# Performance work log

Hardware: AMD Instinct MI355X
Metric: run time of the kernel (lower is better)

The kernel has to match this reference:

```python
import jax, jax.numpy as jnp
import numpy as np

B, S, HID = 2, 2048, 4096
NH, NKV, D = 32, 8, 128  # heads, kv heads, head_dim
GROUPS = NH // NKV
THETA = 10000.0


def _rope_tables():
    inv_freq = 1.0 / (THETA ** (np.arange(0, D, 2, dtype=np.float32) / D))
    pos = np.arange(S, dtype=np.float32)
    freqs = pos[:, None] * inv_freq[None, :]          # [S, D/2]
    emb = np.concatenate([freqs, freqs], axis=-1)      # [S, D]
    cos = np.broadcast_to(np.cos(emb)[None], (B, S, D)).copy()
    sin = np.broadcast_to(np.sin(emb)[None], (B, S, D)).copy()
    return jnp.asarray(cos), jnp.asarray(sin)


def setup_inputs() -> dict:
    key = jax.random.key(0)
    ks = jax.random.split(key, 5)
    hidden_states = jax.random.normal(ks[0], (B, S, HID), dtype=jnp.float32)
    cos, sin = _rope_tables()
    std = 0.02
    Wq = jax.random.normal(ks[1], (NH * D, HID), dtype=jnp.float32) * std
    Wk = jax.random.normal(ks[2], (NKV * D, HID), dtype=jnp.float32) * std
    Wv = jax.random.normal(ks[3], (NKV * D, HID), dtype=jnp.float32) * std
    Wo = jax.random.normal(ks[4], (HID, NH * D), dtype=jnp.float32) * std
    return {"hidden_states": hidden_states, "cos": cos, "sin": sin,
            "Wq": Wq, "Wk": Wk, "Wv": Wv, "Wo": Wo}


def _rotate_half(x):
    x1, x2 = jnp.split(x, 2, axis=-1)
    return jnp.concatenate([-x2, x1], axis=-1)


def reference(hidden_states, cos, sin, Wq, Wk, Wv, Wo):
    b, s, _ = hidden_states.shape
    # QKV projections (no bias; attention_bias=False)
    q = (hidden_states @ Wq.T).reshape(b, s, NH, D).transpose(0, 2, 1, 3)    # [B,NH,S,D]
    k = (hidden_states @ Wk.T).reshape(b, s, NKV, D).transpose(0, 2, 1, 3)   # [B,NKV,S,D]
    v = (hidden_states @ Wv.T).reshape(b, s, NKV, D).transpose(0, 2, 1, 3)
    # RoPE (HF apply_rotary_pos_emb: cos/sin unsqueezed at head dim)
    c = cos[:, None, :, :]
    sn = sin[:, None, :, :]
    q = q * c + _rotate_half(q) * sn
    k = k * c + _rotate_half(k) * sn
    # GQA repeat_kv
    k = jnp.repeat(k, GROUPS, axis=1)                                        # [B,NH,S,D]
    v = jnp.repeat(v, GROUPS, axis=1)
    # dense evalmode: scores + causal mask + fp32 softmax
    scores = jnp.einsum('bhqd,bhkd->bhqk', q, k) / jnp.sqrt(jnp.float32(D))
    causal = jnp.triu(jnp.ones((s, s), dtype=bool), k=1)                     # True above diag
    scores = jnp.where(causal[None, None], jnp.float32(-jnp.inf), scores)
    attn = jax.nn.softmax(scores.astype(jnp.float32), axis=-1).astype(v.dtype)
    out = jnp.einsum('bhqk,bhkd->bhqd', attn, v)                             # [B,NH,S,D]
    out = out.transpose(0, 2, 1, 3).reshape(b, s, NH * D)
    return out @ Wo.T
```

## Files before the change

### kernel.cpp

```cpp
#include <hip/hip_runtime.h>
#include <hip/hip_bf16.h>

#define DEV __device__ __forceinline__

typedef __attribute__((ext_vector_type(8))) short bf16x8;
typedef __attribute__((ext_vector_type(4))) short s16x4;
typedef __attribute__((ext_vector_type(4))) float f32x4;

constexpr int B_ = 2, S_ = 2048, HID_ = 4096, NH_ = 32, NKV_ = 8, D_ = 128;
constexpr int GROUPS_ = NH_ / NKV_;
constexpr float QSCALE_ = 0.08838834764831845f * 1.4426950408889634f;

DEV unsigned short f2bf(float x) {
    union { float f; unsigned int u; } v; v.f = x;
    unsigned int r = v.u + 0x7fffu + ((v.u >> 16) & 1u);
    return (unsigned short)(r >> 16);
}

DEV f32x4 mfma16(bf16x8 a, bf16x8 b, f32x4 c) {
    return __builtin_amdgcn_mfma_f32_16x16x32_bf16(a, b, c, 0, 0, 0);
}

DEV void gll16(const void* g, void* l) {
    __builtin_amdgcn_global_load_lds(
        (const __attribute__((address_space(1))) unsigned int*)g,
        (__attribute__((address_space(3))) unsigned int*)l, 16, 0, 0);
}

__global__ __launch_bounds__(256) void cast_all_k(
    const float* __restrict__ s0, const float* __restrict__ s1,
    const float* __restrict__ s2, const float* __restrict__ s3,
    const float* __restrict__ s4,
    unsigned short* __restrict__ d0, unsigned short* __restrict__ d1,
    unsigned short* __restrict__ d2, unsigned short* __restrict__ d3,
    unsigned short* __restrict__ d4)
{
    int bb = blockIdx.x;
    const float* s; unsigned short* d; int off;
    if      (bb < 8192)  { s = s0; d = d0; off = bb; }
    else if (bb < 16384) { s = s1; d = d1; off = bb - 8192; }
    else if (bb < 18432) { s = s2; d = d2; off = bb - 16384; }
    else if (bb < 20480) { s = s3; d = d3; off = bb - 18432; }
    else                 { s = s4; d = d4; off = bb - 20480; }
    size_t i = ((size_t)off * 256 + threadIdx.x) * 8;
    const f32x4* sp = (const f32x4*)(s + i);
    f32x4 a = sp[0], b = sp[1];
    bf16x8 o;
    o[0] = (short)f2bf(a[0]); o[1] = (short)f2bf(a[1]);
    o[2] = (short)f2bf(a[2]); o[3] = (short)f2bf(a[3]);
    o[4] = (short)f2bf(b[0]); o[5] = (short)f2bf(b[1]);
    o[6] = (short)f2bf(b[2]); o[7] = (short)f2bf(b[3]);
    *(bf16x8*)(d + i) = o;
}

template<int EPI>
__global__ __launch_bounds__(512, 2) void gemm256_k(
    const unsigned short* __restrict__ A, const unsigned short* __restrict__ Bw,
    float* __restrict__ Cf, unsigned short* __restrict__ Qo,
    const float* __restrict__ cosT, const float* __restrict__ sinT,
    int M, int N, int K)
{
    __shared__ __align__(16) unsigned short lds[65536];
    const int tid = threadIdx.x, lane = tid & 63;
    const int w = tid >> 6, wm = w >> 2, wn = w & 3;
    const int la = lane & 15, lb = lane >> 4;

    const int nwg = (int)gridDim.x;
    const int cpx = nwg >> 3;
    const int bid = (int)blockIdx.x;
    const int sw = (bid & 7) * cpx + (bid >> 3);
    const int ntn = N >> 8;
    const int bm = (sw / ntn) << 8, bn = (sw % ntn) << 8;

    const int srow = tid >> 3;
    const int scol8 = (tid & 7) ^ (srow & 7);
    const size_t rK = (size_t)K;
    const unsigned short* gA = A + (size_t)(bm + srow) * rK + scol8 * 8;
    const unsigned short* gB = Bw + (size_t)(bn + srow) * rK + scol8 * 8;

#define STAGE_A_H0(buf, kt) { gll16(gA + (size_t)(kt),            &lds[(buf)*16384 + tid*8]); \
                              gll16(gA + (size_t)(kt) + 128*rK,   &lds[(buf)*16384 + 8192 + tid*8]); }
#define STAGE_A_H1(buf, kt) { gll16(gA + (size_t)(kt) + 64*rK,    &lds[(buf)*16384 + 4096 + tid*8]); \
                              gll16(gA + (size_t)(kt) + 192*rK,   &lds[(buf)*16384 + 12288 + tid*8]); }
#define STAGE_B_H0(buf, kt) { gll16(gB + (size_t)(kt),            &lds[32768 + (buf)*16384 + tid*8]); \
                              gll16(gB + (size_t)(kt) + 64*rK,    &lds[32768 + (buf)*16384 + 4096 + tid*8]); }
#define STAGE_B_H1(buf, kt) { gll16(gB + (size_t)(kt) + 128*rK,   &lds[32768 + (buf)*16384 + 8192 + tid*8]); \
                              gll16(gB + (size_t)(kt) + 192*rK,   &lds[32768 + (buf)*16384 + 12288 + tid*8]); }
#define SB0() __builtin_amdgcn_sched_barrier(0)

    f32x4 acc[8][4];
#pragma unroll
    for (int m = 0; m < 8; ++m)
#pragma unroll
        for (int j = 0; j < 4; ++j) acc[m][j] = f32x4{0.f, 0.f, 0.f, 0.f};

    auto rdA = [&](int buf, int m, int kk) -> bf16x8 {
        int r = wm * 128 + m * 16 + la;
        int slot = (kk * 4 + lb) ^ (la & 7);
        return *(const bf16x8*)&lds[buf * 16384 + r * 64 + slot * 8];
    };
    auto rdB = [&](int buf, int j, int kk) -> bf16x8 {
        int r = (wn + 4 * j) * 16 + la;
        int slot = (kk * 4 + lb) ^ (la & 7);
        return *(const bf16x8*)&lds[32768 + buf * 16384 + r * 64 + slot * 8];
    };

    STAGE_A_H0(0, 0); STAGE_B_H0(0, 0); STAGE_B_H1(0, 0); STAGE_A_H1(0, 0);

    bf16x8 af[4][2], b01[2][2], b23[2][2];
    int cur = 0;
    const int nt = K >> 6;
    for (int t = 0; t < nt; ++t) {
        const bool pre = (t + 1 < nt);
        const int kn = (t + 1) << 6;
        const int nb = cur ^ 1;
        asm volatile("s_waitcnt vmcnt(2)" ::: "memory");
        SB0(); __builtin_amdgcn_s_barrier(); SB0();
#pragma unroll
        for (int m = 0; m < 4; ++m)
#pragma unroll
            for (int kk = 0; kk < 2; ++kk) af[m][kk] = rdA(cur, m, kk);
#pragma unroll
        for (int j = 0; j < 2; ++j)
#pragma unroll
            for (int kk = 0; kk < 2; ++kk) b01[j][kk] = rdB(cur, j, kk);
        if (pre) STAGE_A_H0(nb, kn);
        __builtin_amdgcn_s_setprio(1);
#pragma unroll
        for (int kk = 0; kk < 2; ++kk)
#pragma unroll
            for (int m = 0; m < 4; ++m)
#pragma unroll
                for (int j = 0; j < 2; ++j)
                    acc[m][j] = mfma16(af[m][kk], b01[j][kk], acc[m][j]);
        __builtin_amdgcn_s_setprio(0);
        SB0(); __builtin_amdgcn_s_barrier(); SB0();
#pragma unroll
        for (int j = 0; j < 2; ++j)
#pragma unroll
            for (int kk = 0; kk < 2; ++kk) b23[j][kk] = rdB(cur, j + 2, kk);
        if (pre) STAGE_B_H0(nb, kn);
        __builtin_amdgcn_s_setprio(1);
#pragma unroll
        for (int kk = 0; kk < 2; ++kk)
#pragma unroll
            for (int m = 0; m < 4; ++m)
#pragma unroll
                for (int j = 0; j < 2; ++j)
                    acc[m][j + 2] = mfma16(af[m][kk], b23[j][kk], acc[m][j + 2]);
        __builtin_amdgcn_s_setprio(0);
        if (pre) { asm volatile("s_waitcnt vmcnt(4)" ::: "memory"); }
        else     { asm volatile("s_waitcnt vmcnt(0)" ::: "memory"); }
        SB0(); __builtin_amdgcn_s_barrier(); SB0();
#pragma unroll
        for (int m = 0; m < 4; ++m)
#pragma unroll
            for (int kk = 0; kk < 2; ++kk) af[m][kk] = rdA(cur, m + 4, kk);
        if (pre) STAGE_B_H1(nb, kn);
        __builtin_amdgcn_s_setprio(1);
#pragma unroll
        for (int kk = 0; kk < 2; ++kk)
#pragma unroll
            for (int m = 0; m < 4; ++m)
#pragma unroll
                for (int j = 0; j < 2; ++j)
                    acc[m + 4][j + 2] = mfma16(af[m][kk], b23[j][kk], acc[m + 4][j + 2]);
        __builtin_amdgcn_s_setprio(0);
        SB0(); __builtin_amdgcn_s_barrier(); SB0();
        if (pre) STAGE_A_H1(nb, kn);
        __builtin_amdgcn_s_setprio(1);
#pragma unroll
        for (int kk = 0; kk < 2; ++kk)
#pragma unroll
            for (int m = 0; m < 4; ++m)
#pragma unroll
                for (int j = 0; j < 2; ++j)
                    acc[m + 4][j] = mfma16(af[m][kk], b01[j][kk], acc[m + 4][j]);
        __builtin_amdgcn_s_setprio(0);
        cur ^= 1;
    }
#undef STAGE_A_H0
#undef STAGE_A_H1
#undef STAGE_B_H0
#undef STAGE_B_H1

    const int srow0 = bm + wm * 128;
    if constexpr (EPI == 0) {
#pragma unroll
        for (int m = 0; m < 8; ++m)
#pragma unroll
            for (int j = 0; j < 4; ++j) {
                int col = bn + (wn + 4 * j) * 16 + la;
#pragma unroll
                for (int r = 0; r < 4; ++r)
                    Cf[(size_t)(srow0 + m * 16 + lb * 4 + r) * N + col] = acc[m][j][r];
            }
    } else {
        const int hbase = bn >> 7;
        const int d = wn * 16 + la;
#pragma unroll
        for (int m = 0; m < 8; ++m) {
#pragma unroll
            for (int r = 0; r < 4; ++r) {
                int row = srow0 + m * 16 + lb * 4 + r;
                float cv = cosT[(size_t)row * D_ + d];
                float sv = sinT[(size_t)row * D_ + d];
#pragma unroll
                for (int p = 0; p < 2; ++p) {
                    float x1 = acc[m][p * 2 + 0][r], x2 = acc[m][p * 2 + 1][r];
                    unsigned short* o = Qo + (size_t)row * (NH_ * D_) + (hbase + p) * D_ + d;
                    o[0]  = f2bf((x1 * cv - x2 * sv) * QSCALE_);
                    o[64] = f2bf((x2 * cv + x1 * sv) * QSCALE_);
                }
            }
        }
    }
}

__global__ __launch_bounds__(512, 4) void gemm_kv_k(
    const unsigned short* __restrict__ A, const unsigned short* __restrict__ Bw,
    unsigned short* __restrict__ Ko, unsigned short* __restrict__ Vo,
    const float* __restrict__ cosT, const float* __restrict__ sinT,
    int M, int K)
{
    __shared__ __align__(16) unsigned short lds[32768];
    const int tid = threadIdx.x, lane = tid & 63;
    const int w = tid >> 6, wm = w >> 2, wn = w & 3;
    const int la = lane & 15, lb = lane >> 4;

    const int nwg = (int)gridDim.x;
    const int cpx = nwg >> 3;
    const int bid = (int)blockIdx.x;
    const int sw = (bid & 7) * cpx + (bid >> 3);
    const int ntn = 2048 >> 7;
    const int bm = (sw / ntn) << 7, bn = (sw % ntn) << 7;

    const int srow = tid >> 3;
    const int scol8 = (tid & 7) ^ (srow & 7);
    const size_t rK = (size_t)K;
    const unsigned short* gA = A + (size_t)(bm + srow) * rK + scol8 * 8;
    const unsigned short* gB = Bw + (size_t)(bn + srow) * rK + scol8 * 8;

#define KV_STG_A(buf, kt)  { gll16(gA + (size_t)(kt),          &lds[(buf)*8192 + tid*8]); \
                             gll16(gA + (size_t)(kt) + 64*rK,  &lds[(buf)*8192 + 4096 + tid*8]); }
#define KV_STG_B0(buf, kt)   gll16(gB + (size_t)(kt),          &lds[16384 + (buf)*8192 + tid*8])
#define KV_STG_B1(buf, kt)   gll16(gB + (size_t)(kt) + 64*rK,  &lds[16384 + (buf)*8192 + 4096 + tid*8])

    f32x4 acc[4][2];
#pragma unroll
    for (int m = 0; m < 4; ++m)
#pragma unroll
        for (int j = 0; j < 2; ++j) acc[m][j] = f32x4{0.f, 0.f, 0.f, 0.f};

    auto rdA = [&](int buf, int m, int kk) -> bf16x8 {
        int r = wm * 64 + m * 16 + la;
        int slot = (kk * 4 + lb) ^ (la & 7);
        return *(const bf16x8*)&lds[buf * 8192 + r * 64 + slot * 8];
    };
    auto rdB = [&](int buf, int j, int kk) -> bf16x8 {
        int r = (wn + 4 * j) * 16 + la;
        int slot = (kk * 4 + lb) ^ (la & 7);
        return *(const bf16x8*)&lds[16384 + buf * 8192 + r * 64 + slot * 8];
    };

    KV_STG_A(0, 0); KV_STG_B0(0, 0); KV_STG_B1(0, 0);

    bf16x8 af[4][2], bf0[2], bf1[2];
    int cur = 0;
    const int nt = K >> 6;
    for (int t = 0; t < nt; ++t) {
        const bool pre = (t + 1 < nt);
        const int kn = (t + 1) << 6;
        const int nb = cur ^ 1;
        asm volatile("s_waitcnt vmcnt(1)" ::: "memory");
        SB0(); __builtin_amdgcn_s_barrier(); SB0();
#pragma unroll
        for (int m = 0; m < 4; ++m)
#pragma unroll
            for (int kk = 0; kk < 2; ++kk) af[m][kk] = rdA(cur, m, kk);
#pragma unroll
        for (int kk = 0; kk < 2; ++kk) bf0[kk] = rdB(cur, 0, kk);
        if (pre) { KV_STG_A(nb, kn); KV_STG_B0(nb, kn); }
        __builtin_amdgcn_s_setprio(1);
#pragma unroll
        for (int kk = 0; kk < 2; ++kk)
#pragma unroll
            for (int m = 0; m < 4; ++m)
                acc[m][0] = mfma16(af[m][kk], bf0[kk], acc[m][0]);
        __builtin_amdgcn_s_setprio(0);
        if (pre) { asm volatile("s_waitcnt vmcnt(3)" ::: "memory"); }
        else     { asm volatile("s_waitcnt vmcnt(0)" ::: "memory"); }
        SB0(); __builtin_amdgcn_s_barrier(); SB0();
#pragma unroll
        for (int kk = 0; kk < 2; ++kk) bf1[kk] = rdB(cur, 1, kk);
        if (pre) KV_STG_B1(nb, kn);
        __builtin_amdgcn_s_setprio(1);
#pragma unroll
        for (int kk = 0; kk < 2; ++kk)
#pragma unroll
            for (int m = 0; m < 4; ++m)
                acc[m][1] = mfma16(af[m][kk], bf1[kk], acc[m][1]);
        __builtin_amdgcn_s_setprio(0);
        cur ^= 1;
    }
#undef KV_STG_A
#undef KV_STG_B0
#undef KV_STG_B1
#undef SB0

    const int rbase = bm + wm * 64;
    if (bn < 1024) {
        const int hbase = bn >> 7;
        const int d = wn * 16 + la;
#pragma unroll
        for (int m = 0; m < 4; ++m)
#pragma unroll
            for (int r = 0; r < 4; ++r) {
                int row = rbase + m * 16 + lb * 4 + r;
                float cv = cosT[(size_t)row * D_ + d];
                float sv = sinT[(size_t)row * D_ + d];
                float x1 = acc[m][0][r], x2 = acc[m][1][r];
                unsigned short* o = Ko + (size_t)row * (NKV_ * D_) + hbase * D_ + d;
                o[0]  = f2bf(x1 * cv - x2 * sv);
                o[64] = f2bf(x2 * cv + x1 * sv);
            }
    } else {
        const int kv = (bn - 1024) >> 7;
#pragma unroll
        for (int m = 0; m < 4; ++m) {
            int row = rbase + m * 16 + lb * 4;
            int b = row >> 11, s = row & (S_ - 1);
#pragma unroll
            for (int j = 0; j < 2; ++j) {
                int d = (wn + 4 * j) * 16 + la;
                s16x4 pk;
#pragma unroll
                for (int r = 0; r < 4; ++r) pk[r] = (short)f2bf(acc[m][j][r]);
                *(s16x4*)&Vo[((size_t)(b * NKV_ + kv) * D_ + d) * S_ + s] = pk;
            }
        }
    }
}

template<int EPI, bool ABF16>
__global__ __launch_bounds__(256) void gemm_legacy_k(
    const void* __restrict__ Ap, const float* __restrict__ Bp,
    void* __restrict__ Cp, const float* __restrict__ cosT,
    const float* __restrict__ sinT, int M, int N, int K, float scale)
{
    constexpr int LDT = 40;
    __shared__ __align__(16) unsigned short Asm[128 * LDT];
    __shared__ __align__(16) unsigned short Bsm[128 * LDT];
    const int tid = threadIdx.x;
    const int lane = tid & 63;
    const int w = tid >> 6;
    const int la = lane & 15, lb = lane >> 4;
    const int ntn = N >> 7;
    const int bm = (int)(blockIdx.x / ntn) << 7;
    const int bn = (int)(blockIdx.x % ntn) << 7;

    f32x4 acc[2][8];
#pragma unroll
    for (int i = 0; i < 2; ++i)
#pragma unroll
        for (int j = 0; j < 8; ++j) acc[i][j] = f32x4{0.f, 0.f, 0.f, 0.f};

    for (int kt = 0; kt < K; kt += 32) {
        if constexpr (!ABF16) {
#pragma unroll
            for (int it = 0; it < 4; ++it) {
                int idx = it * 256 + tid;
                int r = idx >> 3, c = (idx & 7) << 2;
                const float* g = (const float*)Ap + (size_t)(bm + r) * K + kt + c;
                f32x4 v = *(const f32x4*)g;
                union { unsigned long long q; unsigned short u[4]; } pk;
                pk.u[0] = f2bf(v[0]); pk.u[1] = f2bf(v[1]);
                pk.u[2] = f2bf(v[2]); pk.u[3] = f2bf(v[3]);
                *(unsigned long long*)&Asm[r * LDT + c] = pk.q;
            }
        } else {
#pragma unroll
            for (int it = 0; it < 2; ++it) {
                int idx = it * 256 + tid;
                int r = idx >> 2, c = (idx & 3) << 3;
                const unsigned short* g =
                    (const unsigned short*)Ap + (size_t)(bm + r) * K + kt + c;
                *(bf16x8*)&Asm[r * LDT + c] = *(const bf16x8*)g;
            }
        }
#pragma unroll
        for (int it = 0; it < 4; ++it) {
            int idx = it * 256 + tid;
            int r = idx >> 3, c = (idx & 7) << 2;
            const float* g = Bp + (size_t)(bn + r) * K + kt + c;
            f32x4 v = *(const f32x4*)g;
            union { unsigned long long q; unsigned short u[4]; } pk;
            pk.u[0] = f2bf(v[0]); pk.u[1] = f2bf(v[1]);
            pk.u[2] = f2bf(v[2]); pk.u[3] = f2bf(v[3]);
            *(unsigned long long*)&Bsm[r * LDT + c] = pk.q;
        }
        __syncthreads();
        bf16x8 af0 = *(bf16x8*)&Asm[(w * 32 + la) * LDT + lb * 8];
        bf16x8 af1 = *(bf16x8*)&Asm[(w * 32 + 16 + la) * LDT + lb * 8];
#pragma unroll
        for (int nb = 0; nb < 8; ++nb) {
            bf16x8 bfr = *(bf16x8*)&Bsm[(nb * 16 + la) * LDT + lb * 8];
            acc[0][nb] = mfma16(af0, bfr, acc[0][nb]);
            acc[1][nb] = mfma16(af1, bfr, acc[1][nb]);
        }
        __syncthreads();
    }

    const int rbase = bm + w * 32;
    if constexpr (EPI == 0) {
        float* C = (float*)Cp;
#pragma unroll
        for (int mf = 0; mf < 2; ++mf)
#pragma unroll
            for (int nb = 0; nb < 8; ++nb)
#pragma unroll
                for (int r = 0; r < 4; ++r)
                    C[(size_t)(rbase + mf * 16 + lb * 4 + r) * N + bn + nb * 16 + la] =
                        acc[mf][nb][r];
    } else if constexpr (EPI == 1) {
        unsigned short* C = (unsigned short*)Cp;
#pragma unroll
        for (int mf = 0; mf < 2; ++mf) {
#pragma unroll
            for (int r = 0; r < 4; ++r) {
                int m = rbase + mf * 16 + lb * 4 + r;
                const float* cb = cosT + (size_t)m * D_;
                const float* sb = sinT + (size_t)m * D_;
#pragma unroll
                for (int nb = 0; nb < 4; ++nb) {
                    int d = nb * 16 + la;
                    float c = cb[d], s = sb[d];
                    float x1 = acc[mf][nb][r], x2 = acc[mf][nb + 4][r];
                    C[(size_t)m * N + bn + d]      = f2bf((x1 * c - x2 * s) * scale);
                    C[(size_t)m * N + bn + d + 64] = f2bf((x2 * c + x1 * s) * scale);
                }
            }
        }
    } else {
        unsigned short* C = (unsigned short*)Cp;
#pragma unroll
        for (int mf = 0; mf < 2; ++mf)
#pragma unroll
            for (int nb = 0; nb < 8; ++nb)
#pragma unroll
                for (int r = 0; r < 4; ++r) {
                    int m = rbase + mf * 16 + lb * 4 + r;
                    int b = m >> 11, s = m & (S_ - 1);
                    int n = bn + nb * 16 + la;
                    int kv = n >> 7, d = n & 127;
                    C[(((size_t)b * NKV_ + kv) * D_ + d) * S_ + s] =
                        f2bf(acc[mf][nb][r]);
                }
    }
}

__global__ __launch_bounds__(256, 2) void attn2_k(
    const unsigned short* __restrict__ Qw,
    const unsigned short* __restrict__ Kw,
    const unsigned short* __restrict__ Vt,
    unsigned short* __restrict__ Ow)
{
    constexpr int LDP = 72;
    __shared__ __align__(16) unsigned short Ksm[64 * 128];
    __shared__ __align__(16) unsigned short Vsm[128 * 64];
    __shared__ __align__(16) unsigned short Psm[4][32 * LDP];
    const int tid = threadIdx.x, lane = tid & 63, w = tid >> 6;
    const int la = lane & 15, lb = lane >> 4;
    const int blk = blockIdx.x;
    const int qbi = (S_ / 128 - 1) - (blk >> 6);
    const int bh = blk & 63;
    const int b = bh >> 5, h = bh & 31;
    const int kvh = h >> 2;
    const int qb = qbi * 128;
    const int qw0 = qb + w * 32;

    bf16x8 fq[2][4];
    const unsigned short* qp =
        Qw + ((size_t)(b * S_ + qw0 + la) * NH_ + h) * D_ + lb * 8;
#pragma unroll
    for (int mq = 0; mq < 2; ++mq)
#pragma unroll
        for (int kc = 0; kc < 4; ++kc)
            fq[mq][kc] = *(const bf16x8*)(qp + (size_t)mq * 16 * NH_ * D_ + kc * 32);

    float m_[2], l_[2];
    f32x4 oacc[8][2];
    m_[0] = m_[1] = -__builtin_inff();
    l_[0] = l_[1] = 0.f;
#pragma unroll
    for (int db = 0; db < 8; ++db)
#pragma unroll
        for (int mq = 0; mq < 2; ++mq) oacc[db][mq] = f32x4{0.f, 0.f, 0.f, 0.f};

    const int ntiles = (qb + 128) >> 6;
    for (int t = 0; t < ntiles; ++t) {
        const int kv0 = t << 6;
        {
            const int rb = tid >> 4, sl = tid & 15;
#pragma unroll
            for (int it = 0; it < 4; ++it) {
                int row = it * 16 + rb;
                int cc = sl ^ (row & 7);
                const unsigned short* g =
                    Kw + ((size_t)(b * S_ + kv0 + row) * NKV_ + kvh) * D_ + cc * 8;
                gll16(g, &Ksm[(it * 256 + tid) * 8]);
            }
        }
        {
            const int rb = tid >> 3, sl = tid & 7;
#pragma unroll
            for (int it = 0; it < 4; ++it) {
                int row = it * 32 + rb;
                int cc = sl ^ (row & 7);
                const unsigned short* g =
                    Vt + ((size_t)(b * NKV_ + kvh) * D_ + row) * S_ + kv0 + cc * 8;
                gll16(g, &Vsm[(it * 256 + tid) * 8]);
            }
        }
        __syncthreads();

        if (kv0 < qw0 + 32) {
            f32x4 sacc[4][2];
#pragma unroll
            for (int nk = 0; nk < 4; ++nk)
#pragma unroll
                for (int mq = 0; mq < 2; ++mq) sacc[nk][mq] = f32x4{0.f, 0.f, 0.f, 0.f};
#pragma unroll
            for (int kc = 0; kc < 4; ++kc) {
#pragma unroll
                for (int nk = 0; nk < 4; ++nk) {
                    int row = nk * 16 + la;
                    int slot = (kc * 4 + lb) ^ (la & 7);
                    bf16x8 fk = *(const bf16x8*)&Ksm[row * 128 + slot * 8];
#pragma unroll
                    for (int mq = 0; mq < 2; ++mq)
                        sacc[nk][mq] = mfma16(fk, fq[mq][kc], sacc[nk][mq]);
                }
            }
            const bool diag = (kv0 + 63 > qw0);
            float pv[4][2][4];
            float pm[2];
#pragma unroll
            for (int mq = 0; mq < 2; ++mq) {
                int q = qw0 + mq * 16 + la;
                float mx = -__builtin_inff();
#pragma unroll
                for (int nk = 0; nk < 4; ++nk)
#pragma unroll
                    for (int r = 0; r < 4; ++r) {
                        float s = sacc[nk][mq][r];
                        if (diag) {
                            int k = kv0 + nk * 16 + lb * 4 + r;
                            s = (k <= q) ? s : -__builtin_inff();
                        }
                        pv[nk][mq][r] = s;
                        mx = fmaxf(mx, s);
                    }
                mx = fmaxf(mx, __shfl_xor(mx, 16));
                mx = fmaxf(mx, __shfl_xor(mx, 32));
                pm[mq] = mx;
            }
            const bool upd =
                __any((pm[0] > m_[0] + 8.f) || (pm[1] > m_[1] + 8.f));
            if (upd) {
#pragma unroll
                for (int mq = 0; mq < 2; ++mq) {
                    float mn = fmaxf(m_[mq], pm[mq]);
                    float fac = exp2f(m_[mq] - mn);
                    m_[mq] = mn;
                    l_[mq] *= fac;
#pragma unroll
                    for (int db = 0; db < 8; ++db) oacc[db][mq] *= fac;
                }
            }
            float tsum[2] = {0.f, 0.f};
#pragma unroll
            for (int nk = 0; nk < 4; ++nk)
#pragma unroll
                for (int mq = 0; mq < 2; ++mq)
#pragma unroll
                    for (int r = 0; r < 4; ++r) {
                        float p = exp2f(pv[nk][mq][r] - m_[mq]);
                        pv[nk][mq][r] = p;
                        tsum[mq] += p;
                    }
#pragma unroll
            for (int mq = 0; mq < 2; ++mq) {
                float s = tsum[mq];
                s += __shfl_xor(s, 16);
                s += __shfl_xor(s, 32);
                l_[mq] += s;
            }

            unsigned short* pp = &Psm[w][0];
#pragma unroll
            for (int nk = 0; nk < 4; ++nk)
#pragma unroll
                for (int mq = 0; mq < 2; ++mq) {
                    s16x4 pk;
#pragma unroll
                    for (int r = 0; r < 4; ++r) pk[r] = (short)f2bf(pv[nk][mq][r]);
                    *(s16x4*)&pp[(mq * 16 + la) * LDP + nk * 16 + lb * 4] = pk;
                }
            bf16x8 fp[2][2];
#pragma unroll
            for (int mq = 0; mq < 2; ++mq)
#pragma unroll
                for (int ks = 0; ks < 2; ++ks)
                    fp[mq][ks] =
                        *(const bf16x8*)&pp[(mq * 16 + la) * LDP + ks * 32 + lb * 8];
#pragma unroll
            for (int ks = 0; ks < 2; ++ks)
#pragma unroll
                for (int db = 0; db < 8; ++db) {
                    int row = db * 16 + la;
                    int slot = (ks * 4 + lb) ^ (la & 7);
                    bf16x8 fv = *(const bf16x8*)&Vsm[row * 64 + slot * 8];
#pragma unroll
                    for (int mq = 0; mq < 2; ++mq)
                        oacc[db][mq] = mfma16(fv, fp[mq][ks], oacc[db][mq]);
                }
        }
        __syncthreads();
    }

#pragma unroll
    for (int mq = 0; mq < 2; ++mq) {
        float rl = 1.f / l_[mq];
        int q = qw0 + mq * 16 + la;
#pragma unroll
        for (int db = 0; db < 8; ++db) {
            f32x4 o = oacc[db][mq];
            s16x4 pk;
#pragma unroll
            for (int r = 0; r < 4; ++r) pk[r] = (short)f2bf(o[r] * rl);
            int d = db * 16 + lb * 4;
            *(s16x4*)(Ow + (size_t)(b * S_ + q) * (NH_ * D_) + h * D_ + d) = pk;
        }
    }
}

extern "C" void kernel_launch(void* const* d_in, const int* in_sizes, int n_in,
                              void* d_out, int out_size, void* d_ws, size_t ws_size,
                              hipStream_t stream) {
    const float* hs   = (const float*)d_in[0];
    const float* cosT = (const float*)d_in[1];
    const float* sinT = (const float*)d_in[2];
    const float* Wq   = (const float*)d_in[3];
    const float* Wk   = (const float*)d_in[4];
    const float* Wv   = (const float*)d_in[5];
    const float* Wo   = (const float*)d_in[6];

    constexpr size_t Qn  = (size_t)B_ * S_ * NH_ * D_;
    constexpr size_t Kn  = (size_t)B_ * S_ * NKV_ * D_;
    constexpr size_t Hn  = (size_t)B_ * S_ * HID_;
    constexpr size_t Wqn = (size_t)NH_ * D_ * HID_;
    constexpr size_t Wkn = (size_t)NKV_ * D_ * HID_;

    unsigned short* Qws   = (unsigned short*)d_ws;
    unsigned short* Kws   = Qws + Qn;
    unsigned short* Vtws  = Kws + Kn;
    unsigned short* AOws  = Vtws + Kn;
    unsigned short* hsb   = AOws + Qn;
    unsigned short* Wqkvb = hsb + Hn;
    unsigned short* Wob   = Wqkvb + Wqn + 2 * Wkn;
    constexpr size_t need = (Qn + 2 * Kn + Qn + Hn + Wqn + 2 * Wkn + Wqn) * 2;

    const int M = B_ * S_;
    dim3 blk(256);

    if (ws_size >= need) {
        cast_all_k<<<dim3(28672), blk, 0, stream>>>(
            hs, Wq, Wk, Wv, Wo,
            hsb, Wqkvb, Wqkvb + Wqn, Wqkvb + Wqn + Wkn, Wob);

        gemm256_k<1><<<dim3((M / 256) * (HID_ / 256)), dim3(512), 0, stream>>>(
            hsb, Wqkvb, nullptr, Qws, cosT, sinT, M, HID_, HID_);
        gemm_kv_k<<<dim3((M / 128) * (2048 / 128)), dim3(512), 0, stream>>>(
            hsb, Wqkvb + Wqn, Kws, Vtws, cosT, sinT, M, HID_);
        attn2_k<<<dim3(B_ * NH_ * (S_ / 128)), blk, 0, stream>>>(Qws, Kws, Vtws, AOws);
        gemm256_k<0><<<dim3((M / 256) * (HID_ / 256)), dim3(512), 0, stream>>>(
            AOws, Wob, (float*)d_out, nullptr, nullptr, nullptr, M, HID_, NH_ * D_);
    } else {
        unsigned short* Qf = (unsigned short*)d_ws;
        unsigned short* Kf = Qf + Qn;
        unsigned short* Vf = Kf + Kn;
        unsigned short* AOf = Vf + Kn;
        gemm_legacy_k<1, false><<<dim3((M / 128) * (NH_ * D_ / 128)), blk, 0, stream>>>(
            hs, Wq, Qf, cosT, sinT, M, NH_ * D_, HID_, QSCALE_);
        gemm_legacy_k<1, false><<<dim3((M / 128) * (NKV_ * D_ / 128)), blk, 0, stream>>>(
            hs, Wk, Kf, cosT, sinT, M, NKV_ * D_, HID_, 1.0f);
        gemm_legacy_k<3, false><<<dim3((M / 128) * (NKV_ * D_ / 128)), blk, 0, stream>>>(
            hs, Wv, Vf, nullptr, nullptr, M, NKV_ * D_, HID_, 0.f);
        attn2_k<<<dim3(B_ * NH_ * (S_ / 128)), blk, 0, stream>>>(Qf, Kf, Vf, AOf);
        gemm_legacy_k<0, true><<<dim3((M / 128) * (HID_ / 128)), blk, 0, stream>>>(
            AOf, Wo, (float*)d_out, nullptr, nullptr, M, HID_, NH_ * D_, 0.f);
    }
}
```

Before: 479.5 us.

## Double-buffer K/V tiles in attention and keep P in registers

The attention kernel now double-buffers its K and V shared-memory tiles. It prefetches the next tile with async global-to-LDS loads while the current tile is computed, using a partial vmcnt wait and raw barriers in place of the load-then-__syncthreads pattern. The P matrix no longer goes through a per-wave LDS round trip. Its bf16 fragments are packed directly in registers, and the V fragment reads are split into two 4-element loads to match the register layout of the C/D accumulator. The cost is twice the K/V LDS footprint and reliance on a hand-tuned vmcnt count, which could affect occupancy and correctness if the load count changes.

```diff
diff --git a/kernel.cpp b/kernel.cpp
--- a/kernel.cpp
+++ b/kernel.cpp
@@ -245,6 +245,7 @@
                              gll16(gA + (size_t)(kt) + 64*rK,  &lds[(buf)*8192 + 4096 + tid*8]); }
 #define KV_STG_B0(buf, kt)   gll16(gB + (size_t)(kt),          &lds[16384 + (buf)*8192 + tid*8])
 #define KV_STG_B1(buf, kt)   gll16(gB + (size_t)(kt) + 64*rK,  &lds[16384 + (buf)*8192 + 4096 + tid*8])
+#define SB0() __builtin_amdgcn_sched_barrier(0)
 
     f32x4 acc[4][2];
 #pragma unroll
@@ -459,16 +460,14 @@
     }
 }
 
-__global__ __launch_bounds__(256, 2) void attn2_k(
+__global__ __launch_bounds__(256, 2) void attn3_k(
     const unsigned short* __restrict__ Qw,
     const unsigned short* __restrict__ Kw,
     const unsigned short* __restrict__ Vt,
     unsigned short* __restrict__ Ow)
 {
-    constexpr int LDP = 72;
-    __shared__ __align__(16) unsigned short Ksm[64 * 128];
-    __shared__ __align__(16) unsigned short Vsm[128 * 64];
-    __shared__ __align__(16) unsigned short Psm[4][32 * LDP];
+    __shared__ __align__(16) unsigned short Ksm[2][64 * 128];
+    __shared__ __align__(16) unsigned short Vsm[2][128 * 64];
     const int tid = threadIdx.x, lane = tid & 63, w = tid >> 6;
     const int la = lane & 15, lb = lane >> 4;
     const int blk = blockIdx.x;
@@ -497,32 +496,39 @@
 #pragma unroll
         for (int mq = 0; mq < 2; ++mq) oacc[db][mq] = f32x4{0.f, 0.f, 0.f, 0.f};
 
+    const int krb = tid >> 4, ksl = tid & 15;
+    const int vrb = tid >> 3, vsl = tid & 7;
+    const unsigned short* kbase = Kw + ((size_t)b * S_ * NKV_ + kvh) * D_;
+    const unsigned short* vbase = Vt + ((size_t)(b * NKV_ + kvh) * D_) * S_;
+
+#define STAGE_KV(buf, kv0) {                                                   \
+    _Pragma("unroll")                                                          \
+    for (int it = 0; it < 4; ++it) {                                           \
+        int row = it * 16 + krb;                                               \
+        int cc = ksl ^ (row & 7);                                              \
+        gll16(kbase + (size_t)(kv0 + row) * NKV_ * D_ + cc * 8,                \
+              &Ksm[buf][(it * 256 + tid) * 8]);                                \
+    }                                                                          \
+    _Pragma("unroll")                                                          \
+    for (int it = 0; it < 4; ++it) {                                           \
+        int row = it * 32 + vrb;                                               \
+        int cc = vsl ^ (row & 7);                                              \
+        gll16(vbase + (size_t)row * S_ + (kv0) + cc * 8,                       \
+              &Vsm[buf][(it * 256 + tid) * 8]);                                \
+    }                                                                          \
+}
+#define SB0() __builtin_amdgcn_sched_barrier(0)
+
+    STAGE_KV(0, 0);
+    int cur = 0;
     const int ntiles = (qb + 128) >> 6;
     for (int t = 0; t < ntiles; ++t) {
         const int kv0 = t << 6;
-        {
-            const int rb = tid >> 4, sl = tid & 15;
-#pragma unroll
-            for (int it = 0; it < 4; ++it) {
-                int row = it * 16 + rb;
-                int cc = sl ^ (row & 7);
-                const unsigned short* g =
-                    Kw + ((size_t)(b * S_ + kv0 + row) * NKV_ + kvh) * D_ + cc * 8;
-                gll16(g, &Ksm[(it * 256 + tid) * 8]);
-            }
-        }
-        {
-            const int rb = tid >> 3, sl = tid & 7;
-#pragma unroll
-            for (int it = 0; it < 4; ++it) {
-                int row = it * 32 + rb;
-                int cc = sl ^ (row & 7);
-                const unsigned short* g =
-                    Vt + ((size_t)(b * NKV_ + kvh) * D_ + row) * S_ + kv0 + cc * 8;
-                gll16(g, &Vsm[(it * 256 + tid) * 8]);
-            }
-        }
-        __syncthreads();
+        const bool pre = (t + 1 < ntiles);
+        if (pre) STAGE_KV(cur ^ 1, kv0 + 64);
+        if (pre) { asm volatile("s_waitcnt vmcnt(8)" ::: "memory"); }
+        else     { asm volatile("s_waitcnt vmcnt(0)" ::: "memory"); }
+        SB0(); __builtin_amdgcn_s_barrier(); SB0();
 
         if (kv0 < qw0 + 32) {
             f32x4 sacc[4][2];
@@ -536,7 +542,7 @@
                 for (int nk = 0; nk < 4; ++nk) {
                     int row = nk * 16 + la;
                     int slot = (kc * 4 + lb) ^ (la & 7);
-                    bf16x8 fk = *(const bf16x8*)&Ksm[row * 128 + slot * 8];
+                    bf16x8 fk = *(const bf16x8*)&Ksm[cur][row * 128 + slot * 8];
 #pragma unroll
                     for (int mq = 0; mq < 2; ++mq)
                         sacc[nk][mq] = mfma16(fk, fq[mq][kc], sacc[nk][mq]);
@@ -596,38 +602,41 @@
                 s += __shfl_xor(s, 32);
                 l_[mq] += s;
             }
-
-            unsigned short* pp = &Psm[w][0];
-#pragma unroll
-            for (int nk = 0; nk < 4; ++nk)
-#pragma unroll
-                for (int mq = 0; mq < 2; ++mq) {
-                    s16x4 pk;
-#pragma unroll
-                    for (int r = 0; r < 4; ++r) pk[r] = (short)f2bf(pv[nk][mq][r]);
-                    *(s16x4*)&pp[(mq * 16 + la) * LDP + nk * 16 + lb * 4] = pk;
+            union { bf16x8 v; __hip_bfloat162 h[4]; } fp[2][2];
+#pragma unroll
+            for (int mq = 0; mq < 2; ++mq)
+#pragma unroll
+                for (int ks = 0; ks < 2; ++ks) {
+                    fp[mq][ks].h[0] = __float22bfloat162_rn(
+                        float2{pv[2 * ks][mq][0], pv[2 * ks][mq][1]});
+                    fp[mq][ks].h[1] = __float22bfloat162_rn(
+                        float2{pv[2 * ks][mq][2], pv[2 * ks][mq][3]});
+                    fp[mq][ks].h[2] = __float22bfloat162_rn(
+                        float2{pv[2 * ks + 1][mq][0], pv[2 * ks + 1][mq][1]});
+                    fp[mq][ks].h[3] = __float22bfloat162_rn(
+                        float2{pv[2 * ks + 1][mq][2], pv[2 * ks + 1][mq][3]});
                 }
-            bf16x8 fp[2][2];
-#pragma unroll
-            for (int mq = 0; mq < 2; ++mq)
-#pragma unroll
-                for (int ks = 0; ks < 2; ++ks)
-                    fp[mq][ks] =
-                        *(const bf16x8*)&pp[(mq * 16 + la) * LDP + ks * 32 + lb * 8];
+            const int lbh = lb >> 1, lbo = (lb & 1) * 4;
 #pragma unroll
             for (int ks = 0; ks < 2; ++ks)
 #pragma unroll
                 for (int db = 0; db < 8; ++db) {
                     int row = db * 16 + la;
-                    int slot = (ks * 4 + lb) ^ (la & 7);
-                    bf16x8 fv = *(const bf16x8*)&Vsm[row * 64 + slot * 8];
+                    int rx = row & 7;
+                    const unsigned short* vb = &Vsm[cur][row * 64];
+                    s16x4 v0 = *(const s16x4*)&vb[((ks * 4 + lbh) ^ rx) * 8 + lbo];
+                    s16x4 v1 = *(const s16x4*)&vb[((ks * 4 + 2 + lbh) ^ rx) * 8 + lbo];
+                    bf16x8 fv = __builtin_shufflevector(v0, v1, 0, 1, 2, 3, 4, 5, 6, 7);
 #pragma unroll
                     for (int mq = 0; mq < 2; ++mq)
-                        oacc[db][mq] = mfma16(fv, fp[mq][ks], oacc[db][mq]);
+                        oacc[db][mq] = mfma16(fv, fp[mq][ks].v, oacc[db][mq]);
                 }
         }
-        __syncthreads();
-    }
+        SB0(); __builtin_amdgcn_s_barrier(); SB0();
+        cur ^= 1;
+    }
+#undef STAGE_KV
+#undef SB0
 
 #pragma unroll
     for (int mq = 0; mq < 2; ++mq) {
@@ -683,7 +692,7 @@
             hsb, Wqkvb, nullptr, Qws, cosT, sinT, M, HID_, HID_);
         gemm_kv_k<<<dim3((M / 128) * (2048 / 128)), dim3(512), 0, stream>>>(
             hsb, Wqkvb + Wqn, Kws, Vtws, cosT, sinT, M, HID_);
-        attn2_k<<<dim3(B_ * NH_ * (S_ / 128)), blk, 0, stream>>>(Qws, Kws, Vtws, AOws);
+        attn3_k<<<dim3(B_ * NH_ * (S_ / 128)), blk, 0, stream>>>(Qws, Kws, Vtws, AOws);
         gemm256_k<0><<<dim3((M / 256) * (HID_ / 256)), dim3(512), 0, stream>>>(
             AOws, Wob, (float*)d_out, nullptr, nullptr, nullptr, M, HID_, NH_ * D_);
     } else {
@@ -697,7 +706,7 @@
             hs, Wk, Kf, cosT, sinT, M, NKV_ * D_, HID_, 1.0f);
         gemm_legacy_k<3, false><<<dim3((M / 128) * (NKV_ * D_ / 128)), blk, 0, stream>>>(
             hs, Wv, Vf, nullptr, nullptr, M, NKV_ * D_, HID_, 0.f);
-        attn2_k<<<dim3(B_ * NH_ * (S_ / 128)), blk, 0, stream>>>(Qf, Kf, Vf, AOf);
+        attn3_k<<<dim3(B_ * NH_ * (S_ / 128)), blk, 0, stream>>>(Qf, Kf, Vf, AOf);
         gemm_legacy_k<0, true><<<dim3((M / 128) * (HID_ / 128)), blk, 0, stream>>>(
             AOf, Wo, (float*)d_out, nullptr, nullptr, M, HID_, NH_ * D_, 0.f);
     }
```

After: 474.2 us. Within noise of the previous version (-1.1%).
